# Performance work log

Measured on AMD Instinct MI355X. Metric: run time of the kernel, lower is better.

## Reference

```python
import jax, jax.numpy as jnp
import numpy as np


def _attend(q, k, v, scale):
    # q: [B,H,Lq,D], k/v: [B,H,Lk,D]
    logits = jnp.einsum('bhqd,bhkd->bhqk', q, k) * scale
    a = jax.nn.softmax(logits, axis=-1)
    return jnp.einsum('bhqk,bhkd->bhqd', a, v)


def _merge_heads(x):
    # [B,H,L,D] -> [B,L,H*D]
    B, H, L, D = x.shape
    return x.transpose(0, 2, 1, 3).reshape(B, L, H * D)


def setup_inputs() -> dict:
    key = jax.random.key(0)
    ks = jax.random.split(key, 4)
    B, N, C = 64, 384, 768
    x_v = jax.random.normal(ks[0], (B, N, C), dtype=jnp.float32)
    x_i = jax.random.normal(ks[1], (B, N, C), dtype=jnp.float32)
    w_qkv = jax.random.normal(ks[2], (3 * C, C), dtype=jnp.float32) * (C ** -0.5)
    b_qkv = jnp.zeros((3 * C,), dtype=jnp.float32)
    w_proj = jax.random.normal(ks[3], (C, C), dtype=jnp.float32) * (C ** -0.5)
    b_proj = jnp.zeros((C,), dtype=jnp.float32)
    return {"x_v": x_v, "x_i": x_i, "w_qkv": w_qkv, "b_qkv": b_qkv,
            "w_proj": w_proj, "b_proj": b_proj, "t_h": 8, "t_w": 8, "lens_s": 256}


def reference(x_v, x_i, w_qkv, b_qkv, w_proj, b_proj, t_h, t_w, lens_s):
    B, N, C = x_v.shape
    H = 12
    D = C // H
    scale = D ** -0.5
    L_mt = t_h * t_w * 2

    x = jnp.concatenate([x_v, x_i], axis=0)              # [2B,N,C]
    qkv = x @ w_qkv.T + b_qkv                            # [2B,N,3C]
    qkv = qkv.reshape(2 * B, N, 3, H, D).transpose(2, 0, 3, 1, 4)  # [3,2B,H,N,D]
    q, k, v = qkv[0], qkv[1], qkv[2]
    qV, qI = q[:B], q[B:]
    kV, kI = k[:B], k[B:]
    vV, vI = v[:B], v[B:]

    q_mt_V, q_s_V = qV[:, :, :L_mt], qV[:, :, L_mt:]
    k_mt_V, k_s_V = kV[:, :, :L_mt], kV[:, :, L_mt:]
    v_mt_V, v_s_V = vV[:, :, :L_mt], vV[:, :, L_mt:]
    q_mt_I, q_s_I = qI[:, :, :L_mt], qI[:, :, L_mt:]
    k_mt_I, k_s_I = kI[:, :, :L_mt], kI[:, :, L_mt:]
    v_mt_I, v_s_I = vI[:, :, :L_mt], vI[:, :, L_mt:]

    k_mt = jnp.concatenate([k_mt_V, k_mt_I], axis=2)     # [B,H,2*L_mt,D]
    v_mt = jnp.concatenate([v_mt_V, v_mt_I], axis=2)

    # template self-attention per modality
    x_mt_V = _merge_heads(_attend(q_mt_V, k_mt_V, v_mt_V, scale))  # [B,L_mt,C]
    x_mt_I = _merge_heads(_attend(q_mt_I, k_mt_I, v_mt_I, scale))

    # search attends to both-modality templates + own-modality search
    x_s_V = _merge_heads(_attend(q_s_V,
                                 jnp.concatenate([k_mt, k_s_V], axis=2),
                                 jnp.concatenate([v_mt, v_s_V], axis=2), scale))
    x_s_I = _merge_heads(_attend(q_s_I,
                                 jnp.concatenate([k_mt, k_s_I], axis=2),
                                 jnp.concatenate([v_mt, v_s_I], axis=2), scale))

    x_V = jnp.concatenate([x_mt_V, x_s_V], axis=1)       # [B,N,C]
    x_I = jnp.concatenate([x_mt_I, x_s_I], axis=1)
    out = jnp.concatenate([x_V, x_I], axis=0) @ w_proj.T + b_proj  # [2B,N,C]
    return out[:B], out[B:]
```

## Files before the change

kernel.cpp:

```cpp
#include <hip/hip_runtime.h>


typedef unsigned short u16;
typedef unsigned int   u32;
typedef float f32x4 __attribute__((ext_vector_type(4)));
typedef short bfrag  __attribute__((ext_vector_type(8)));

__device__ __forceinline__ f32x4 mfma16(bfrag a, bfrag b, f32x4 c) {
  return __builtin_amdgcn_mfma_f32_16x16x32_bf16(a, b, c, 0, 0, 0);
}
__device__ __forceinline__ u16 bf16_rn(float f) {
  u32 u = __builtin_bit_cast(u32, f);
  return (u16)((u + 0x7fffu + ((u >> 16) & 1u)) >> 16);
}
__device__ __forceinline__ u32 pack_rn(float a, float b) {
  u32 ua = __builtin_bit_cast(u32, a), ub = __builtin_bit_cast(u32, b);
  ua = (ua + 0x7fffu + ((ua >> 16) & 1u)) >> 16;
  ub = (ub + 0x7fffu + ((ub >> 16) & 1u)) & 0xffff0000u;
  return ua | ub;
}

__device__ __forceinline__ void gll16(const u16* g, u16* l) {
  __builtin_amdgcn_global_load_lds((const __attribute__((address_space(1))) void*)g,
                                   (__attribute__((address_space(3))) void*)l, 16, 0, 0);
}

__global__ __launch_bounds__(256)
void convert_kernel(const float* __restrict__ xv, const float* __restrict__ xi,
                    const float* __restrict__ wq, const float* __restrict__ wp,
                    u16* __restrict__ Ah, u16* __restrict__ Bh, u16* __restrict__ Ph) {
  const size_t NA = (size_t)49152 * 768, NB = (size_t)2304 * 768, NP = (size_t)768 * 768;
  const size_t HALF = (size_t)24576 * 768;
  size_t tid = (size_t)blockIdx.x * 256 + threadIdx.x;
  size_t stride = (size_t)gridDim.x * 256;
  for (size_t i = tid; i < NA / 8; i += stride) {
    size_t e = i * 8;
    const float* s = (e < HALF) ? (xv + e) : (xi + (e - HALF));
    float4 a = ((const float4*)s)[0], b = ((const float4*)s)[1];
    ((uint4*)Ah)[i] = make_uint4(pack_rn(a.x, a.y), pack_rn(a.z, a.w),
                                 pack_rn(b.x, b.y), pack_rn(b.z, b.w));
  }
  for (size_t i = tid; i < NB / 8; i += stride) {
    float4 a = ((const float4*)(wq + i * 8))[0], b = ((const float4*)(wq + i * 8))[1];
    ((uint4*)Bh)[i] = make_uint4(pack_rn(a.x, a.y), pack_rn(a.z, a.w),
                                 pack_rn(b.x, b.y), pack_rn(b.z, b.w));
  }
  for (size_t i = tid; i < NP / 8; i += stride) {
    float4 a = ((const float4*)(wp + i * 8))[0], b = ((const float4*)(wp + i * 8))[1];
    ((uint4*)Ph)[i] = make_uint4(pack_rn(a.x, a.y), pack_rn(a.z, a.w),
                                 pack_rn(b.x, b.y), pack_rn(b.z, b.w));
  }
}

template <int EPI, int NBLK>
__global__ __launch_bounds__(256, 3)
void gemm_bf16(const u16* __restrict__ Ag, const u16* __restrict__ Bg,
               const float* __restrict__ bias,
               u16* __restrict__ qo, u16* __restrict__ ko, u16* __restrict__ vo,
               float* __restrict__ outp) {
  __shared__ u16 AT[128 * 64];
  __shared__ u16 BT[128 * 64];

  const int cpx = gridDim.x >> 3;
  const int bid = (blockIdx.x & 7) * cpx + (blockIdx.x >> 3);
  const int nb = bid % NBLK, mb = bid / NBLK;
  const int t = threadIdx.x;
  const int lane = t & 63;
  const int wv = t >> 6, wm = wv >> 1, wn = wv & 1;
  const int l15 = lane & 15, lg = lane >> 4;

  const int lr = lane >> 3;
  const int gs = (lane & 7) ^ lr;
  const u16* asrc = Ag + ((size_t)(mb * 128 + wv * 32 + lr)) * 768 + gs * 8;
  const u16* bsrc = Bg + ((size_t)(nb * 128 + wv * 32 + lr)) * 768 + gs * 8;

  f32x4 acc[4][4];
#pragma unroll
  for (int i = 0; i < 4; i++)
#pragma unroll
    for (int j = 0; j < 4; j++) acc[i][j] = (f32x4){0.f, 0.f, 0.f, 0.f};

  for (int k0 = 0; k0 < 768; k0 += 64) {
#pragma unroll
    for (int i = 0; i < 4; i++) {
      gll16(asrc + (size_t)i * 8 * 768 + k0, AT + (wv * 32 + i * 8) * 64);
      gll16(bsrc + (size_t)i * 8 * 768 + k0, BT + (wv * 32 + i * 8) * 64);
    }
    __syncthreads();

#pragma unroll
    for (int ks = 0; ks < 2; ks++) {
      bfrag af[4], bf[4];
#pragma unroll
      for (int ms = 0; ms < 4; ms++) {
        int row = wm * 64 + ms * 16 + l15;
        af[ms] = *(const bfrag*)&AT[row * 64 + (((ks * 4 + lg) ^ (row & 7)) * 8)];
      }
#pragma unroll
      for (int ns = 0; ns < 4; ns++) {
        int row = wn * 64 + ns * 16 + l15;
        bf[ns] = *(const bfrag*)&BT[row * 64 + (((ks * 4 + lg) ^ (row & 7)) * 8)];
      }
#pragma unroll
      for (int ms = 0; ms < 4; ms++)
#pragma unroll
        for (int ns = 0; ns < 4; ns++)
          acc[ms][ns] = mfma16(af[ms], bf[ns], acc[ms][ns]);
    }
    __syncthreads();
  }

#pragma unroll
  for (int ms = 0; ms < 4; ms++) {
#pragma unroll
    for (int ns = 0; ns < 4; ns++) {
      int n = nb * 128 + wn * 64 + ns * 16 + l15;
      float bv = bias[n];
#pragma unroll
      for (int r = 0; r < 4; r++) {
        int m = mb * 128 + wm * 64 + ms * 16 + lg * 4 + r;
        float f = acc[ms][ns][r] + bv;
        if constexpr (EPI == 0) {
          int which = n / 768;
          int hh = (n % 768) / 64;
          int d = n % 64;
          int b2i = m / 384, tok = m % 384;
          int bhn = b2i * 12 + hh;
          if (which == 0) {
            qo[((size_t)bhn * 384 + tok) * 64 + d] = bf16_rn(f * 0.125f);
          } else if (which == 1) {
            ko[((size_t)bhn * 384 + tok) * 64 + d] = bf16_rn(f);
          } else {
            vo[((size_t)bhn * 64 + d) * 384 + tok] = bf16_rn(f);
          }
        } else {
          outp[(size_t)m * 768 + n] = f;
        }
      }
    }
  }
}

__global__ __launch_bounds__(256, 2)
void attn_kernel(const u16* __restrict__ q, const u16* __restrict__ k,
                 const u16* __restrict__ vT, u16* __restrict__ oh) {
  __shared__ u16 KL[64 * 64];
  __shared__ u16 VL[64 * 64];
  __shared__ float PL[4][16 * 68];

  const int cpx = gridDim.x >> 3;
  const int bid = (blockIdx.x & 7) * cpx + (blockIdx.x >> 3);
  const int qb = bid % 6, bh = bid / 6;
  const int b2i = bh / 12, hh = bh % 12;
  const int q0 = qb * 64;
  const int t = threadIdx.x;
  const int lane = t & 63, wv = t >> 6;
  const int l15 = lane & 15, lg = lane >> 4;
  const int rs = t >> 2, gq = (t & 3) * 2;

  const u16* qp = q + ((size_t)bh * 384 + q0 + wv * 16 + l15) * 64 + lg * 8;
  bfrag qf0 = *(const bfrag*)(qp);
  bfrag qf1 = *(const bfrag*)(qp + 32);

  f32x4 o[4];
#pragma unroll
  for (int i = 0; i < 4; i++) o[i] = (f32x4){0.f, 0.f, 0.f, 0.f};
  float m_run[4], l_run[4];
#pragma unroll
  for (int r = 0; r < 4; r++) { m_run[r] = -1e30f; l_run[r] = 0.f; }

  const int nblk = (q0 < 128) ? 2 : 8;

  for (int kb = 0; kb < nblk; kb++) {
    int src_bh, row0;
    if (q0 < 128)      { src_bh = bh;                          row0 = kb * 64; }
    else if (kb < 2)   { src_bh = (b2i & 63) * 12 + hh;        row0 = kb * 64; }
    else if (kb < 4)   { src_bh = ((b2i & 63) + 64) * 12 + hh; row0 = (kb - 2) * 64; }
    else               { src_bh = bh;                          row0 = 128 + (kb - 4) * 64; }

    {
      const u16* krow = k + ((size_t)src_bh * 384 + row0 + rs) * 64 + gq * 8;
      uint4 ka = *(const uint4*)(krow);
      uint4 kbv = *(const uint4*)(krow + 8);
      *(uint4*)&KL[rs * 64 + ((gq ^ (rs & 7)) * 8)] = ka;
      *(uint4*)&KL[rs * 64 + (((gq + 1) ^ (rs & 7)) * 8)] = kbv;
      const u16* vrow = vT + ((size_t)src_bh * 64 + rs) * 384 + row0 + gq * 8;
      uint4 va = *(const uint4*)(vrow);
      uint4 vb = *(const uint4*)(vrow + 8);
      *(uint4*)&VL[rs * 64 + ((gq ^ (rs & 7)) * 8)] = va;
      *(uint4*)&VL[rs * 64 + (((gq + 1) ^ (rs & 7)) * 8)] = vb;
    }
    __syncthreads();

    f32x4 S[4];
#pragma unroll
    for (int nt = 0; nt < 4; nt++) S[nt] = (f32x4){0.f, 0.f, 0.f, 0.f};
#pragma unroll
    for (int nt = 0; nt < 4; nt++) {
      int row = nt * 16 + l15;
      bfrag k0f = *(const bfrag*)&KL[row * 64 + ((lg ^ (row & 7)) * 8)];
      bfrag k1f = *(const bfrag*)&KL[row * 64 + (((4 + lg) ^ (row & 7)) * 8)];
      S[nt] = mfma16(qf0, k0f, S[nt]);
      S[nt] = mfma16(qf1, k1f, S[nt]);
    }

    float ps[4];
#pragma unroll
    for (int r = 0; r < 4; r++) {
      float v = fmaxf(fmaxf(S[0][r], S[1][r]), fmaxf(S[2][r], S[3][r]));
      v = fmaxf(v, __shfl_xor(v, 1));
      v = fmaxf(v, __shfl_xor(v, 2));
      v = fmaxf(v, __shfl_xor(v, 4));
      v = fmaxf(v, __shfl_xor(v, 8));
      float nm = fmaxf(m_run[r], v);
      float fac = __expf(m_run[r] - nm);
      m_run[r] = nm;
      l_run[r] *= fac;
      o[0][r] *= fac; o[1][r] *= fac; o[2][r] *= fac; o[3][r] *= fac;
      ps[r] = 0.f;
    }
#pragma unroll
    for (int nt = 0; nt < 4; nt++)
#pragma unroll
      for (int r = 0; r < 4; r++) {
        float p = __expf(S[nt][r] - m_run[r]);
        ps[r] += p;
        PL[wv][(lg * 4 + r) * 68 + nt * 16 + l15] = p;
      }
#pragma unroll
    for (int r = 0; r < 4; r++) {
      float v = ps[r];
      v += __shfl_xor(v, 1); v += __shfl_xor(v, 2);
      v += __shfl_xor(v, 4); v += __shfl_xor(v, 8);
      l_run[r] += v;
    }
    asm volatile("s_waitcnt lgkmcnt(0)" ::: "memory");

    bfrag pf[2];
#pragma unroll
    for (int ks = 0; ks < 2; ks++) {
      const float* pr = &PL[wv][l15 * 68 + lg * 8 + ks * 32];
      float4 x0 = *(const float4*)(pr);
      float4 x1 = *(const float4*)(pr + 4);
      union { bfrag v; u32 w[4]; } pu;
      pu.w[0] = pack_rn(x0.x, x0.y);
      pu.w[1] = pack_rn(x0.z, x0.w);
      pu.w[2] = pack_rn(x1.x, x1.y);
      pu.w[3] = pack_rn(x1.z, x1.w);
      pf[ks] = pu.v;
    }
#pragma unroll
    for (int dt = 0; dt < 4; dt++) {
      int row = dt * 16 + l15;
      bfrag v0f = *(const bfrag*)&VL[row * 64 + ((lg ^ (row & 7)) * 8)];
      bfrag v1f = *(const bfrag*)&VL[row * 64 + (((4 + lg) ^ (row & 7)) * 8)];
      o[dt] = mfma16(pf[0], v0f, o[dt]);
      o[dt] = mfma16(pf[1], v1f, o[dt]);
    }
    __syncthreads();
  }

#pragma unroll
  for (int r = 0; r < 4; r++) l_run[r] = 1.f / l_run[r];
#pragma unroll
  for (int dt = 0; dt < 4; dt++)
#pragma unroll
    for (int r = 0; r < 4; r++) {
      float f = o[dt][r] * l_run[r];
      int tok = q0 + wv * 16 + lg * 4 + r;
      int col = hh * 64 + dt * 16 + l15;
      oh[((size_t)b2i * 384 + tok) * 768 + col] = bf16_rn(f);
    }
}

extern "C" void kernel_launch(void* const* d_in, const int* in_sizes, int n_in,
                              void* d_out, int out_size, void* d_ws, size_t ws_size,
                              hipStream_t stream) {
  const float* xv    = (const float*)d_in[0];
  const float* xi    = (const float*)d_in[1];
  const float* wqkv  = (const float*)d_in[2];
  const float* bqkv  = (const float*)d_in[3];
  const float* wproj = (const float*)d_in[4];
  const float* bproj = (const float*)d_in[5];
  float* outp = (float*)d_out;

  const size_t SZ = (size_t)1536 * 384 * 64;
  const size_t NB = (size_t)2304 * 768;
  const size_t NP = (size_t)768 * 768;
  const size_t WS_NEED = (SZ + NB + NP + 3 * SZ) * sizeof(u16);
  if (ws_size < WS_NEED) {
    hipMemsetAsync(d_out, 0, (size_t)out_size * sizeof(float), stream);
    return;
  }
  u16* Ah = (u16*)d_ws;
  u16* Bh = Ah + SZ;
  u16* Ph = Bh + NB;
  u16* q_ = Ph + NP;
  u16* k_ = q_ + SZ;
  u16* v_ = k_ + SZ;
  u16* oh = Ah;

  convert_kernel<<<dim3(1024), 256, 0, stream>>>(xv, xi, wqkv, wproj, Ah, Bh, Ph);
  gemm_bf16<0, 18><<<dim3(384 * 18), 256, 0, stream>>>(Ah, Bh, bqkv, q_, k_, v_, nullptr);
  attn_kernel<<<dim3(1536 * 6), 256, 0, stream>>>(q_, k_, v_, oh);
  gemm_bf16<1, 6><<<dim3(384 * 6), 256, 0, stream>>>(oh, Ph, bproj, nullptr, nullptr, nullptr, outp);
}
```

Measured before the change: 843.5 us.

## Replace GEMM with 256x256 double-buffered 8-wave phased pipeline kernel

Replaces the 128x128 single-buffered bf16 GEMM with a 512-thread, 256x256-tile kernel. Global-to-LDS tile loads for step k+2 are issued into LDS double buffers while MFMAs run on the current tile. Each k-step is split into phases separated by s_barrier and sched_barrier, with s_setprio raised around MFMA blocks and explicit vmcnt waits. The aim is to hide load latency and raise data reuse per tile, at the cost of 128KB of LDS, one block per CU, and fewer blocks for the projection GEMM.

```diff
diff --git a/kernel.cpp b/kernel.cpp
--- a/kernel.cpp
+++ b/kernel.cpp
@@ -19,7 +19,6 @@
   ub = (ub + 0x7fffu + ((ub >> 16) & 1u)) & 0xffff0000u;
   return ua | ub;
 }
-
 __device__ __forceinline__ void gll16(const u16* g, u16* l) {
   __builtin_amdgcn_global_load_lds((const __attribute__((address_space(1))) void*)g,
                                    (__attribute__((address_space(3))) void*)l, 16, 0, 0);
@@ -52,74 +51,123 @@
   }
 }
 
+#define PHASE_BAR() do { __builtin_amdgcn_sched_barrier(0); \
+                         __builtin_amdgcn_s_barrier();      \
+                         __builtin_amdgcn_sched_barrier(0); } while (0)
+
+#define STAGE_A(buf, kt, j) \
+  gll16(aS + (size_t)((j) * 64) * 768 + (kt) * 64, &LA[buf][((j) * 64 + w * 8) * 64])
+#define STAGE_B(buf, kt, j) \
+  gll16(bS + (size_t)((j) * 64) * 768 + (kt) * 64, &LB[buf][((j) * 64 + w * 8) * 64])
+
+#define LOAD_A(buf, s)                                                          \
+  _Pragma("unroll") for (int fr = 0; fr < 4; fr++) {                            \
+    int row = wm * 128 + (s) * 64 + fr * 16 + l15;                              \
+    _Pragma("unroll") for (int kk = 0; kk < 2; kk++)                            \
+      a_[fr][kk] = *(const bfrag*)&LA[buf][row * 64 + (((kk * 4 + lg) ^ (row & 7)) * 8)]; \
+  }
+#define LOAD_B(buf, ns)                                                         \
+  _Pragma("unroll") for (int cf = 0; cf < 2; cf++) {                            \
+    int row = wn * 64 + (ns) * 32 + cf * 16 + l15;                              \
+    _Pragma("unroll") for (int kk = 0; kk < 2; kk++)                            \
+      b_[ns][cf][kk] = *(const bfrag*)&LB[buf][row * 64 + (((kk * 4 + lg) ^ (row & 7)) * 8)]; \
+  }
+#define MFMA_Q(ms, ns)                                                          \
+  do {                                                                          \
+    __builtin_amdgcn_s_setprio(1);                                              \
+    _Pragma("unroll") for (int fr = 0; fr < 4; fr++)                            \
+      _Pragma("unroll") for (int cf = 0; cf < 2; cf++)                          \
+        _Pragma("unroll") for (int kk = 0; kk < 2; kk++)                        \
+          acc[(ms) * 4 + fr][(ns) * 2 + cf] =                                   \
+              mfma16(a_[fr][kk], b_[ns][cf][kk], acc[(ms) * 4 + fr][(ns) * 2 + cf]); \
+    __builtin_amdgcn_s_setprio(0);                                              \
+  } while (0)
+
 template <int EPI, int NBLK>
-__global__ __launch_bounds__(256, 3)
-void gemm_bf16(const u16* __restrict__ Ag, const u16* __restrict__ Bg,
-               const float* __restrict__ bias,
-               u16* __restrict__ qo, u16* __restrict__ ko, u16* __restrict__ vo,
-               float* __restrict__ outp) {
-  __shared__ u16 AT[128 * 64];
-  __shared__ u16 BT[128 * 64];
+__global__ __launch_bounds__(512, 2)
+void gemm_8ph(const u16* __restrict__ Ag, const u16* __restrict__ Bg,
+              const float* __restrict__ bias,
+              u16* __restrict__ qo, u16* __restrict__ ko, u16* __restrict__ vo,
+              float* __restrict__ outp) {
+  __shared__ u16 LA[2][256 * 64];
+  __shared__ u16 LB[2][256 * 64];
 
   const int cpx = gridDim.x >> 3;
   const int bid = (blockIdx.x & 7) * cpx + (blockIdx.x >> 3);
   const int nb = bid % NBLK, mb = bid / NBLK;
   const int t = threadIdx.x;
   const int lane = t & 63;
-  const int wv = t >> 6, wm = wv >> 1, wn = wv & 1;
+  const int w = t >> 6;
+  const int wm = w >> 2, wn = w & 3;
   const int l15 = lane & 15, lg = lane >> 4;
-
-  const int lr = lane >> 3;
-  const int gs = (lane & 7) ^ lr;
-  const u16* asrc = Ag + ((size_t)(mb * 128 + wv * 32 + lr)) * 768 + gs * 8;
-  const u16* bsrc = Bg + ((size_t)(nb * 128 + wv * 32 + lr)) * 768 + gs * 8;
-
-  f32x4 acc[4][4];
-#pragma unroll
-  for (int i = 0; i < 4; i++)
+  const int lr = lane >> 3, gs = (lane & 7) ^ lr;
+
+  const u16* aS = Ag + (size_t)(mb * 256 + w * 8 + lr) * 768 + gs * 8;
+  const u16* bS = Bg + (size_t)(nb * 256 + w * 8 + lr) * 768 + gs * 8;
+
+  f32x4 acc[8][4];
+#pragma unroll
+  for (int i = 0; i < 8; i++)
 #pragma unroll
     for (int j = 0; j < 4; j++) acc[i][j] = (f32x4){0.f, 0.f, 0.f, 0.f};
-
-  for (int k0 = 0; k0 < 768; k0 += 64) {
-#pragma unroll
-    for (int i = 0; i < 4; i++) {
-      gll16(asrc + (size_t)i * 8 * 768 + k0, AT + (wv * 32 + i * 8) * 64);
-      gll16(bsrc + (size_t)i * 8 * 768 + k0, BT + (wv * 32 + i * 8) * 64);
-    }
-    __syncthreads();
-
-#pragma unroll
-    for (int ks = 0; ks < 2; ks++) {
-      bfrag af[4], bf[4];
-#pragma unroll
-      for (int ms = 0; ms < 4; ms++) {
-        int row = wm * 64 + ms * 16 + l15;
-        af[ms] = *(const bfrag*)&AT[row * 64 + (((ks * 4 + lg) ^ (row & 7)) * 8)];
-      }
-#pragma unroll
-      for (int ns = 0; ns < 4; ns++) {
-        int row = wn * 64 + ns * 16 + l15;
-        bf[ns] = *(const bfrag*)&BT[row * 64 + (((ks * 4 + lg) ^ (row & 7)) * 8)];
-      }
-#pragma unroll
-      for (int ms = 0; ms < 4; ms++)
-#pragma unroll
-        for (int ns = 0; ns < 4; ns++)
-          acc[ms][ns] = mfma16(af[ms], bf[ns], acc[ms][ns]);
-    }
-    __syncthreads();
-  }
-
-#pragma unroll
-  for (int ms = 0; ms < 4; ms++) {
-#pragma unroll
-    for (int ns = 0; ns < 4; ns++) {
-      int n = nb * 128 + wn * 64 + ns * 16 + l15;
+  bfrag a_[4][2], b_[2][2][2];
+
+#pragma unroll
+  for (int j = 0; j < 4; j++) { STAGE_A(0, 0, j); }
+#pragma unroll
+  for (int j = 0; j < 4; j++) { STAGE_B(0, 0, j); }
+#pragma unroll
+  for (int j = 0; j < 4; j++) { STAGE_A(1, 1, j); }
+#pragma unroll
+  for (int j = 0; j < 4; j++) { STAGE_B(1, 1, j); }
+  asm volatile("s_waitcnt vmcnt(8)" ::: "memory");
+  PHASE_BAR();
+
+  for (int kt = 0; kt < 12; kt++) {
+    const int cur = kt & 1;
+    const bool pre = (kt < 10);
+    LOAD_A(cur, 0);
+    LOAD_B(cur, 0);
+    PHASE_BAR();
+    MFMA_Q(0, 0);
+    PHASE_BAR();
+    LOAD_B(cur, 1);
+    PHASE_BAR();
+    MFMA_Q(0, 1);
+    PHASE_BAR();
+    LOAD_A(cur, 1);
+    if (pre) {
+#pragma unroll
+      for (int j = 0; j < 4; j++) { STAGE_B(cur, kt + 2, j); }
+    }
+    PHASE_BAR();
+    MFMA_Q(1, 0);
+    PHASE_BAR();
+    if (pre) {
+#pragma unroll
+      for (int j = 0; j < 4; j++) { STAGE_A(cur, kt + 2, j); }
+    }
+    PHASE_BAR();
+    MFMA_Q(1, 1);
+    __builtin_amdgcn_sched_barrier(0);
+    if (kt < 11) {
+      if (pre) asm volatile("s_waitcnt vmcnt(8)" ::: "memory");
+      else     asm volatile("s_waitcnt vmcnt(0)" ::: "memory");
+    }
+    __builtin_amdgcn_s_barrier();
+    __builtin_amdgcn_sched_barrier(0);
+  }
+
+#pragma unroll
+  for (int mr = 0; mr < 8; mr++) {
+#pragma unroll
+    for (int nr = 0; nr < 4; nr++) {
+      int n = nb * 256 + wn * 64 + nr * 16 + l15;
       float bv = bias[n];
 #pragma unroll
       for (int r = 0; r < 4; r++) {
-        int m = mb * 128 + wm * 64 + ms * 16 + lg * 4 + r;
-        float f = acc[ms][ns][r] + bv;
+        int m = mb * 256 + wm * 128 + mr * 16 + lg * 4 + r;
+        float f = acc[mr][nr][r] + bv;
         if constexpr (EPI == 0) {
           int which = n / 768;
           int hh = (n % 768) / 64;
@@ -301,7 +349,7 @@
   u16* oh = Ah;
 
   convert_kernel<<<dim3(1024), 256, 0, stream>>>(xv, xi, wqkv, wproj, Ah, Bh, Ph);
-  gemm_bf16<0, 18><<<dim3(384 * 18), 256, 0, stream>>>(Ah, Bh, bqkv, q_, k_, v_, nullptr);
+  gemm_8ph<0, 9><<<dim3(1728), 512, 0, stream>>>(Ah, Bh, bqkv, q_, k_, v_, nullptr);
   attn_kernel<<<dim3(1536 * 6), 256, 0, stream>>>(q_, k_, v_, oh);
-  gemm_bf16<1, 6><<<dim3(384 * 6), 256, 0, stream>>>(oh, Ph, bproj, nullptr, nullptr, nullptr, outp);
-}
+  gemm_8ph<1, 3><<<dim3(576), 512, 0, stream>>>(oh, Ph, bproj, nullptr, nullptr, nullptr, outp);
+}
```

Result: slower. 883.0 us (+4.7%).

## Compute transposed attention scores in registers, drop LDS staging for K, V and P

Applied to the files above, without the earlier changes.

The attention kernel now computes S^T = K·Q^T, so each lane holds one query column and the softmax row statistics become single scalars reduced over only two shuffles. K and V fragments are loaded straight from global memory into registers, and P is repacked to bf16 with lane shuffles instead of going through shared memory. This removes all LDS traffic and both block barriers, and the launch bound rises to 3 blocks per CU. In exchange every wave re-reads K/V from global or L2 with no sharing across the block, and register pressure goes up.

```diff
diff --git a/kernel.cpp b/kernel.cpp
--- a/kernel.cpp
+++ b/kernel.cpp
@@ -19,7 +19,6 @@
   ub = (ub + 0x7fffu + ((ub >> 16) & 1u)) & 0xffff0000u;
   return ua | ub;
 }
-
 __device__ __forceinline__ void gll16(const u16* g, u16* l) {
   __builtin_amdgcn_global_load_lds((const __attribute__((address_space(1))) void*)g,
                                    (__attribute__((address_space(3))) void*)l, 16, 0, 0);
@@ -141,13 +140,9 @@
   }
 }
 
-__global__ __launch_bounds__(256, 2)
+__global__ __launch_bounds__(256, 3)
 void attn_kernel(const u16* __restrict__ q, const u16* __restrict__ k,
                  const u16* __restrict__ vT, u16* __restrict__ oh) {
-  __shared__ u16 KL[64 * 64];
-  __shared__ u16 VL[64 * 64];
-  __shared__ float PL[4][16 * 68];
-
   const int cpx = gridDim.x >> 3;
   const int bid = (blockIdx.x & 7) * cpx + (blockIdx.x >> 3);
   const int qb = bid % 6, bh = bid / 6;
@@ -156,7 +151,6 @@
   const int t = threadIdx.x;
   const int lane = t & 63, wv = t >> 6;
   const int l15 = lane & 15, lg = lane >> 4;
-  const int rs = t >> 2, gq = (t & 3) * 2;
 
   const u16* qp = q + ((size_t)bh * 384 + q0 + wv * 16 + l15) * 64 + lg * 8;
   bfrag qf0 = *(const bfrag*)(qp);
@@ -165,11 +159,11 @@
   f32x4 o[4];
 #pragma unroll
   for (int i = 0; i < 4; i++) o[i] = (f32x4){0.f, 0.f, 0.f, 0.f};
-  float m_run[4], l_run[4];
-#pragma unroll
-  for (int r = 0; r < 4; r++) { m_run[r] = -1e30f; l_run[r] = 0.f; }
+  float m_run = -1e30f, l_run = 0.f;
 
   const int nblk = (q0 < 128) ? 2 : 8;
+  const int srcA = ((lane & 16) << 1) | l15;
+  const bool lo2 = (lg < 2);
 
   for (int kb = 0; kb < nblk; kb++) {
     int src_bh, row0;
@@ -178,99 +172,83 @@
     else if (kb < 4)   { src_bh = ((b2i & 63) + 64) * 12 + hh; row0 = (kb - 2) * 64; }
     else               { src_bh = bh;                          row0 = 128 + (kb - 4) * 64; }
 
-    {
-      const u16* krow = k + ((size_t)src_bh * 384 + row0 + rs) * 64 + gq * 8;
-      uint4 ka = *(const uint4*)(krow);
-      uint4 kbv = *(const uint4*)(krow + 8);
-      *(uint4*)&KL[rs * 64 + ((gq ^ (rs & 7)) * 8)] = ka;
-      *(uint4*)&KL[rs * 64 + (((gq + 1) ^ (rs & 7)) * 8)] = kbv;
-      const u16* vrow = vT + ((size_t)src_bh * 64 + rs) * 384 + row0 + gq * 8;
-      uint4 va = *(const uint4*)(vrow);
-      uint4 vb = *(const uint4*)(vrow + 8);
-      *(uint4*)&VL[rs * 64 + ((gq ^ (rs & 7)) * 8)] = va;
-      *(uint4*)&VL[rs * 64 + (((gq + 1) ^ (rs & 7)) * 8)] = vb;
-    }
-    __syncthreads();
+    const u16* kb0 = k  + ((size_t)src_bh * 384 + row0) * 64;
+    const u16* vb0 = vT + ((size_t)src_bh * 64) * 384 + row0;
 
     f32x4 S[4];
 #pragma unroll
-    for (int nt = 0; nt < 4; nt++) S[nt] = (f32x4){0.f, 0.f, 0.f, 0.f};
-#pragma unroll
-    for (int nt = 0; nt < 4; nt++) {
-      int row = nt * 16 + l15;
-      bfrag k0f = *(const bfrag*)&KL[row * 64 + ((lg ^ (row & 7)) * 8)];
-      bfrag k1f = *(const bfrag*)&KL[row * 64 + (((4 + lg) ^ (row & 7)) * 8)];
-      S[nt] = mfma16(qf0, k0f, S[nt]);
-      S[nt] = mfma16(qf1, k1f, S[nt]);
-    }
-
-    float ps[4];
-#pragma unroll
-    for (int r = 0; r < 4; r++) {
-      float v = fmaxf(fmaxf(S[0][r], S[1][r]), fmaxf(S[2][r], S[3][r]));
-      v = fmaxf(v, __shfl_xor(v, 1));
-      v = fmaxf(v, __shfl_xor(v, 2));
-      v = fmaxf(v, __shfl_xor(v, 4));
-      v = fmaxf(v, __shfl_xor(v, 8));
-      float nm = fmaxf(m_run[r], v);
-      float fac = __expf(m_run[r] - nm);
-      m_run[r] = nm;
-      l_run[r] *= fac;
-      o[0][r] *= fac; o[1][r] *= fac; o[2][r] *= fac; o[3][r] *= fac;
-      ps[r] = 0.f;
-    }
-#pragma unroll
-    for (int nt = 0; nt < 4; nt++)
-#pragma unroll
-      for (int r = 0; r < 4; r++) {
-        float p = __expf(S[nt][r] - m_run[r]);
-        ps[r] += p;
-        PL[wv][(lg * 4 + r) * 68 + nt * 16 + l15] = p;
-      }
-#pragma unroll
-    for (int r = 0; r < 4; r++) {
-      float v = ps[r];
-      v += __shfl_xor(v, 1); v += __shfl_xor(v, 2);
-      v += __shfl_xor(v, 4); v += __shfl_xor(v, 8);
-      l_run[r] += v;
-    }
-    asm volatile("s_waitcnt lgkmcnt(0)" ::: "memory");
-
-    bfrag pf[2];
-#pragma unroll
-    for (int ks = 0; ks < 2; ks++) {
-      const float* pr = &PL[wv][l15 * 68 + lg * 8 + ks * 32];
-      float4 x0 = *(const float4*)(pr);
-      float4 x1 = *(const float4*)(pr + 4);
-      union { bfrag v; u32 w[4]; } pu;
-      pu.w[0] = pack_rn(x0.x, x0.y);
-      pu.w[1] = pack_rn(x0.z, x0.w);
-      pu.w[2] = pack_rn(x1.x, x1.y);
-      pu.w[3] = pack_rn(x1.z, x1.w);
-      pf[ks] = pu.v;
-    }
+    for (int kt = 0; kt < 4; kt++) {
+      const u16* kr = kb0 + (size_t)(kt * 16 + l15) * 64 + lg * 8;
+      bfrag kf0 = *(const bfrag*)kr;
+      bfrag kf1 = *(const bfrag*)(kr + 32);
+      S[kt] = mfma16(kf0, qf0, (f32x4){0.f, 0.f, 0.f, 0.f});
+      S[kt] = mfma16(kf1, qf1, S[kt]);
+    }
+    bfrag vf0[4], vf1[4];
 #pragma unroll
     for (int dt = 0; dt < 4; dt++) {
-      int row = dt * 16 + l15;
-      bfrag v0f = *(const bfrag*)&VL[row * 64 + ((lg ^ (row & 7)) * 8)];
-      bfrag v1f = *(const bfrag*)&VL[row * 64 + (((4 + lg) ^ (row & 7)) * 8)];
-      o[dt] = mfma16(pf[0], v0f, o[dt]);
-      o[dt] = mfma16(pf[1], v1f, o[dt]);
-    }
-    __syncthreads();
-  }
-
-#pragma unroll
-  for (int r = 0; r < 4; r++) l_run[r] = 1.f / l_run[r];
-#pragma unroll
-  for (int dt = 0; dt < 4; dt++)
-#pragma unroll
-    for (int r = 0; r < 4; r++) {
-      float f = o[dt][r] * l_run[r];
-      int tok = q0 + wv * 16 + lg * 4 + r;
-      int col = hh * 64 + dt * 16 + l15;
-      oh[((size_t)b2i * 384 + tok) * 768 + col] = bf16_rn(f);
-    }
+      const u16* vr = vb0 + (size_t)(dt * 16 + l15) * 384 + lg * 8;
+      vf0[dt] = *(const bfrag*)vr;
+      vf1[dt] = *(const bfrag*)(vr + 32);
+    }
+
+    float mx = S[0][0];
+#pragma unroll
+    for (int kt = 0; kt < 4; kt++)
+#pragma unroll
+      for (int r = 0; r < 4; r++) mx = fmaxf(mx, S[kt][r]);
+    mx = fmaxf(mx, __shfl_xor(mx, 16));
+    mx = fmaxf(mx, __shfl_xor(mx, 32));
+    float nm = fmaxf(m_run, mx);
+    float fac = __expf(m_run - nm);
+    m_run = nm;
+    l_run *= fac;
+#pragma unroll
+    for (int dt = 0; dt < 4; dt++) o[dt] *= fac;
+
+    float ps = 0.f;
+    u32 w[4][2];
+#pragma unroll
+    for (int kt = 0; kt < 4; kt++) {
+      float p0 = __expf(S[kt][0] - nm), p1 = __expf(S[kt][1] - nm);
+      float p2 = __expf(S[kt][2] - nm), p3 = __expf(S[kt][3] - nm);
+      ps += (p0 + p1) + (p2 + p3);
+      w[kt][0] = pack_rn(p0, p1);
+      w[kt][1] = pack_rn(p2, p3);
+    }
+    ps += __shfl_xor(ps, 16);
+    ps += __shfl_xor(ps, 32);
+    l_run += ps;
+
+    union { bfrag v; u32 u[4]; } P0, P1;
+#pragma unroll
+    for (int j = 0; j < 4; j++) {
+      int s = srcA + ((j >> 1) << 4);
+      int sel = j & 1;
+      int a0 = __shfl((int)w[0][sel], s);
+      int a1 = __shfl((int)w[1][sel], s);
+      int a2 = __shfl((int)w[2][sel], s);
+      int a3 = __shfl((int)w[3][sel], s);
+      P0.u[j] = (u32)(lo2 ? a0 : a1);
+      P1.u[j] = (u32)(lo2 ? a2 : a3);
+    }
+
+#pragma unroll
+    for (int dt = 0; dt < 4; dt++) {
+      o[dt] = mfma16(vf0[dt], P0.v, o[dt]);
+      o[dt] = mfma16(vf1[dt], P1.v, o[dt]);
+    }
+  }
+
+  float inv = 1.f / l_run;
+  int tok = q0 + wv * 16 + l15;
+  u16* ob = oh + ((size_t)b2i * 384 + tok) * 768 + hh * 64 + lg * 4;
+#pragma unroll
+  for (int dt = 0; dt < 4; dt++) {
+    u32 w0 = pack_rn(o[dt][0] * inv, o[dt][1] * inv);
+    u32 w1 = pack_rn(o[dt][2] * inv, o[dt][3] * inv);
+    *(uint2*)(ob + dt * 16) = make_uint2(w0, w1);
+  }
 }
 
 extern "C" void kernel_launch(void* const* d_in, const int* in_sizes, int n_in,
```

Result: slower. 1.037 ms (+22.9%).
